# Kernel optimization log

Hardware: AMD Instinct MI355X
Metric: run time of the kernel (lower is better)

## Reference

```python
import jax, jax.numpy as jnp
import numpy as np

B, W, H, A, C, T = 256, 19, 19, 5, 80, 20
DS = 32.0
IOU_THR = 0.5
SCALE_NOOBJ = 0.5
SCALE_OBJ = 5.0
ANCHOR_TRAIN_EPOCHS = 10


def setup_inputs() -> dict:
    key = jax.random.key(0)
    k1, k2, k3, k4, k5, k6 = jax.random.split(key, 6)
    cls_score = jax.random.normal(k1, (B, W, H, A, C), dtype=jnp.float32)
    pred_object = jax.random.normal(k2, (B, W, H, A, 5), dtype=jnp.float32)
    # distinct cells per image -> scatter writes never collide (matches serial loop semantics)
    cell_keys = jax.random.split(k3, B)
    cells = jax.vmap(lambda k: jax.random.permutation(k, W * H)[:T])(cell_keys)  # [B,T]
    ci = (cells // H).astype(jnp.float32)
    cj = (cells % H).astype(jnp.float32)
    off = jax.random.uniform(k4, (B, T, 2), minval=0.2, maxval=0.8)
    wh = jax.random.uniform(k5, (B, T, 2), minval=1.0, maxval=0.9 * W)
    xy = jnp.stack([ci, cj], axis=-1) + off
    true_object = jnp.concatenate([xy, wh], axis=-1) * DS  # image coordinates
    labels = jax.random.randint(k6, (B, T), 0, C)
    true_label = jax.nn.one_hot(labels, C, dtype=jnp.float32)
    # config.anchor_box * fm_width
    anchors = jnp.array([[0.05, 0.07], [0.13, 0.16], [0.22, 0.37], [0.43, 0.26], [0.67, 0.72]],
                        dtype=jnp.float32) * W
    gi, gj = jnp.meshgrid(jnp.arange(W, dtype=jnp.float32), jnp.arange(H, dtype=jnp.float32), indexing='ij')
    fm_cord = jnp.stack([gi, gj], axis=-1)                 # [W,H,2] cell offsets
    fm_size_limit = jnp.full((W, H, 2), float(W), dtype=jnp.float32)
    return {"epoch": 3, "cls_score": cls_score, "pred_object": pred_object,
            "true_object": true_object, "true_label": true_label,
            "anchors": anchors, "fm_cord": fm_cord, "fm_size_limit": fm_size_limit}


def reference(epoch, cls_score, pred_object, true_object, true_label, anchors, fm_cord, fm_size_limit):
    # ---- decode predictions (matches in-place sigmoid decoding) ----
    xy = jax.nn.sigmoid(pred_object[..., :2]) + fm_cord[None, :, :, None, :]
    wh = jax.nn.sigmoid(pred_object[..., 2:4]) * fm_size_limit[None, :, :, None, :]
    conf = jax.nn.sigmoid(pred_object[..., 4])
    pred_dec = jnp.concatenate([xy, wh], axis=-1)          # [B,W,H,A,4]

    # ---- vectorized target assignment (replaces Python b/obj/anchor loops) ----
    to = true_object / DS                                  # [B,T,4] feature-map coords
    ii = jnp.floor(to[..., 0]).astype(jnp.int32)           # [B,T] cell index i
    jj = jnp.floor(to[..., 1]).astype(jnp.int32)           # [B,T] cell index j
    bidx = jnp.arange(B)[:, None]
    pred_cells = pred_dec[bidx, ii, jj]                    # [B,T,A,4] gather

    # center-aligned IoU: only widths/heights matter
    pw, ph = pred_cells[..., 2], pred_cells[..., 3]
    tw, th = to[..., 2][:, :, None], to[..., 3][:, :, None]
    inter = jnp.minimum(pw, tw) * jnp.minimum(ph, th)
    union = pw * ph + tw * th - inter
    iou = inter / union                                    # [B,T,A]
    sel = iou > IOU_THR

    # masked scatter: non-selected rows get an out-of-bounds row index and are dropped
    bb = jnp.broadcast_to(jnp.arange(B)[:, None, None], (B, T, A))
    aa = jnp.broadcast_to(jnp.arange(A)[None, None, :], (B, T, A))
    jj3 = jnp.broadcast_to(jj[:, :, None], (B, T, A))
    ii3 = jnp.where(sel, jnp.broadcast_to(ii[:, :, None], (B, T, A)), W)

    obj_mask = jnp.zeros((B, W, H, A), jnp.float32).at[bb, ii3, jj3, aa].set(1.0, mode='drop')
    iou_buf = jnp.zeros((B, W, H, A), jnp.float32).at[bb, ii3, jj3, aa].set(iou, mode='drop')
    tb_vals = jnp.broadcast_to(to[:, :, None, :], (B, T, A, 4))
    true_bbox = jnp.zeros((B, W, H, A, 4), jnp.float32).at[bb, ii3, jj3, aa].set(tb_vals, mode='drop')
    ts_vals = jnp.broadcast_to(true_label[:, :, None, :], (B, T, A, C))
    true_score = jnp.zeros((B, W, H, A, C), jnp.float32).at[..., -1].set(1.0)
    true_score = true_score.at[bb, ii3, jj3, aa].set(ts_vals, mode='drop')

    # ---- loss terms (MSELoss(reduce=False) == squared error, then mean) ----
    need_prior = 1.0 if epoch < ANCHOR_TRAIN_EPOCHS else 0.0
    noobj_loss = jnp.mean(SCALE_NOOBJ * (1.0 - obj_mask) * 0.5 * conf ** 2)
    obj_loss = jnp.mean(SCALE_OBJ * obj_mask * 0.5 * (conf - iou_buf) ** 2)
    prior_loss = jnp.mean(need_prior * SCALE_OBJ * 0.5 * obj_mask[..., None]
                          * (wh - anchors[None, None, None, :, :]) ** 2)
    true_loss = jnp.mean(SCALE_OBJ * 0.5 * obj_mask[..., None] * (pred_dec - true_bbox) ** 2)
    score_loss = jnp.mean(SCALE_OBJ * 0.5 * (cls_score - true_score) ** 2)
    return (noobj_loss + obj_loss + prior_loss + true_loss + score_loss) / 4.0
```

## Files before the change

### kernel.cpp

```cpp
#include <hip/hip_runtime.h>
#include <math.h>

#define BB 256
#define WD 19
#define HD 19
#define AD 5
#define CD 80
#define TD 20
#define N1 462080
#define NCLS (N1 * CD)
#define NPRED (N1 * 5)

#define NC4 (NCLS / 4)
#define NP4 (NPRED / 4)

#define CLS_BATCHES (NC4 / 1024)
#define PRED_BATCHES (NP4 / 1024)

#define NB_CORR 100
#define NB_CLS  2257
#define NB_PRED 141
#define NBLK (NB_CORR + NB_CLS + NB_PRED)

typedef float f32x4 __attribute__((ext_vector_type(4)));

#define GLOAD(dst, voff, base, imm)                                   \
    asm volatile("global_load_dwordx4 %0, %1, %2 offset:" imm         \
                 : "=v"(dst) : "v"(voff), "s"(base))

__device__ __forceinline__ float sigmoidf_(float x) {
    return 1.0f / (1.0f + expf(-x));
}

#define LOAD_BATCH16(src, b, lane)                                    \
    unsigned o0 = (unsigned)((b) * 1024 + (lane)) * 16u;              \
    unsigned o1 = o0 + 4096u;                                         \
    unsigned o2 = o0 + 8192u;                                         \
    unsigned o3 = o0 + 12288u;                                        \
    f32x4 v0, v1, v2, v3, v4, v5, v6, v7;                             \
    f32x4 v8, v9, v10, v11, v12, v13, v14, v15;                       \
    GLOAD(v0,  o0, src, "0");                                         \
    GLOAD(v1,  o0, src, "1024");                                      \
    GLOAD(v2,  o0, src, "2048");                                      \
    GLOAD(v3,  o0, src, "3072");                                      \
    GLOAD(v4,  o1, src, "0");                                         \
    GLOAD(v5,  o1, src, "1024");                                      \
    GLOAD(v6,  o1, src, "2048");                                      \
    GLOAD(v7,  o1, src, "3072");                                      \
    GLOAD(v8,  o2, src, "0");                                         \
    GLOAD(v9,  o2, src, "1024");                                      \
    GLOAD(v10, o2, src, "2048");                                      \
    GLOAD(v11, o2, src, "3072");                                      \
    GLOAD(v12, o3, src, "0");                                         \
    GLOAD(v13, o3, src, "1024");                                      \
    GLOAD(v14, o3, src, "2048");                                      \
    GLOAD(v15, o3, src, "3072");                                      \
    asm volatile("s_waitcnt vmcnt(0)"                                 \
                 : "+v"(v0), "+v"(v1), "+v"(v2),  "+v"(v3),           \
                   "+v"(v4), "+v"(v5), "+v"(v6),  "+v"(v7),           \
                   "+v"(v8), "+v"(v9), "+v"(v10), "+v"(v11),          \
                   "+v"(v12), "+v"(v13), "+v"(v14), "+v"(v15));

__device__ __forceinline__ void commit_wave(double (*sred)[8], int wib, int lane,
                                            float a0, float a1, float a2, float a3,
                                            float a4, float a5, float a6, float a7) {
    float v[8] = {a0, a1, a2, a3, a4, a5, a6, a7};
    #pragma unroll
    for (int s = 0; s < 8; ++s) {
        #pragma unroll
        for (int off = 32; off > 0; off >>= 1)
            v[s] += __shfl_down(v[s], off, 64);
    }
    if (lane == 0) {
        #pragma unroll
        for (int s = 0; s < 8; ++s) sred[wib][s] = (double)v[s];
    }
}

__global__ void __launch_bounds__(256)
yolo_fused(const float* __restrict__ cls,
           const float* __restrict__ pred,
           const float* __restrict__ tobj,
           const float* __restrict__ tlab,
           const float* __restrict__ anchors,
           const float* __restrict__ fm_cord,
           const float* __restrict__ fm_size,
           double* __restrict__ ws) {
    const int bx = blockIdx.x;
    const int lane = threadIdx.x & 63;
    const int wib = threadIdx.x >> 6;

    __shared__ double sred[4][8];

    if (bx >= NB_CORR && bx < NB_CORR + NB_CLS) {
        const int wave = (bx - NB_CORR) * 4 + wib;
        float sumsq = 0.0f, sum79 = 0.0f;

        if (wave < CLS_BATCHES) {
            const int b = wave;
            LOAD_BATCH16(cls, b, lane);
            const int base20 = (b * 1024 + lane) % 20;
            const f32x4 vv[16] = {v0, v1, v2, v3, v4, v5, v6, v7,
                                  v8, v9, v10, v11, v12, v13, v14, v15};
            #pragma unroll
            for (int k = 0; k < 16; ++k) {
                f32x4 v = vv[k];
                sumsq += v.x * v.x + v.y * v.y + v.z * v.z + v.w * v.w;
                int t = base20 + 4 * k;
                if (t == 19 || t == 39 || t == 59 || t == 79) sum79 += v.w;
            }
        }

        commit_wave(sred, wib, lane, sumsq, sum79, 0.f, 0.f, 0.f, 0.f, 0.f, 0.f);
    } else if (bx >= NB_CORR + NB_CLS) {
        const int wave = (bx - NB_CORR - NB_CLS) * 4 + wib;
        float conf2 = 0.0f;

        {
            const int b = wave;
            LOAD_BATCH16(pred, b, lane);
            const int base5 = (b * 1024 + lane) % 5;
            const f32x4 vv[16] = {v0, v1, v2, v3, v4, v5, v6, v7,
                                  v8, v9, v10, v11, v12, v13, v14, v15};
            #pragma unroll
            for (int k = 0; k < 16; ++k) {
                f32x4 v = vv[k];
                int g5 = (base5 + 4 * k) % 5;
                int kk = (g5 + 4) % 5;
                if (kk < 4) {
                    float x = (kk == 0) ? v.x : (kk == 1) ? v.y
                            : (kk == 2) ? v.z : v.w;
                    float c = sigmoidf_(x);
                    conf2 += c * c;
                }
            }
        }

        if (wave == PRED_BATCHES - 1) {
            int gi = PRED_BATCHES * 1024 + lane;
            float4 v = reinterpret_cast<const float4*>(pred)[gi];
            int kk = (gi + 4) % 5;
            if (kk < 4) {
                float x = (kk == 0) ? v.x : (kk == 1) ? v.y : (kk == 2) ? v.z : v.w;
                float c = sigmoidf_(x);
                conf2 += c * c;
            }
        }

        commit_wave(sred, wib, lane, 0.f, 0.f, conf2, 0.f, 0.f, 0.f, 0.f, 0.f);
    } else {
        const int id = bx * 256 + threadIdx.x;
        float noobj_rm = 0.0f, objs = 0.0f, priors = 0.0f, trues = 0.0f, scorr = 0.0f;

        if (id < BB * TD * AD) {
            int b = id / (TD * AD);
            int r = id % (TD * AD);
            int t = r / AD;
            int a = r % AD;

            const float4 to4 = reinterpret_cast<const float4*>(tobj)[b * TD + t];
            float tox = to4.x * (1.0f / 32.0f);
            float toy = to4.y * (1.0f / 32.0f);
            float tw  = to4.z * (1.0f / 32.0f);
            float th  = to4.w * (1.0f / 32.0f);
            int ii = (int)floorf(tox);
            int jj = (int)floorf(toy);

            const int cell = (b * WD + ii) * HD + jj;
            const float* p = pred + (cell * AD + a) * 5;
            const int fm = (ii * HD + jj) * 2;
            float px = sigmoidf_(p[0]) + fm_cord[fm + 0];
            float py = sigmoidf_(p[1]) + fm_cord[fm + 1];
            float pw = sigmoidf_(p[2]) * fm_size[fm + 0];
            float ph = sigmoidf_(p[3]) * fm_size[fm + 1];
            float conf = sigmoidf_(p[4]);

            float inter = fminf(pw, tw) * fminf(ph, th);
            float uni = pw * ph + tw * th - inter;
            float iou = inter / uni;

            if (iou > 0.5f) {
                noobj_rm = conf * conf;
                objs = (conf - iou) * (conf - iou);
                float aw = anchors[a * 2 + 0];
                float ah = anchors[a * 2 + 1];
                priors = (pw - aw) * (pw - aw) + (ph - ah) * (ph - ah);
                trues = (px - tox) * (px - tox) + (py - toy) * (py - toy)
                      + (pw - tw) * (pw - tw) + (ph - th) * (ph - th);
                const float4* cl4 = reinterpret_cast<const float4*>(cls + (cell * AD + a) * CD);
                const float4* tl4 = reinterpret_cast<const float4*>(tlab + (b * TD + t) * CD);
                float dot = 0.0f;
                float cl79 = 0.0f;
                #pragma unroll 5
                for (int c = 0; c < CD / 4; ++c) {
                    float4 x = cl4[c];
                    float4 y = tl4[c];
                    dot += x.x * y.x + x.y * y.y + x.z * y.z + x.w * y.w;
                    if (c == CD / 4 - 1) cl79 = x.w;
                }
                scorr = 2.0f * cl79 - 2.0f * dot;
            }
        }

        commit_wave(sred, wib, lane, 0.f, 0.f, 0.f, noobj_rm, objs, priors, trues, scorr);
    }

    __syncthreads();
    if (threadIdx.x < 8) {
        ws[bx * 8 + threadIdx.x] = sred[0][threadIdx.x] + sred[1][threadIdx.x]
                                 + sred[2][threadIdx.x] + sred[3][threadIdx.x];
    }
}

__global__ void __launch_bounds__(1024)
yolo_finalize(const double* __restrict__ ws,
              const int* __restrict__ epoch_p,
              float* __restrict__ out) {
    const int lane = threadIdx.x & 63;
    const int wib = threadIdx.x >> 6;
    __shared__ double sh[16][8];

    double acc[8] = {0.0, 0.0, 0.0, 0.0, 0.0, 0.0, 0.0, 0.0};
    for (int b = threadIdx.x; b < NBLK; b += 1024) {
        #pragma unroll
        for (int s = 0; s < 8; ++s) acc[s] += ws[b * 8 + s];
    }
    #pragma unroll
    for (int s = 0; s < 8; ++s) {
        #pragma unroll
        for (int off = 32; off > 0; off >>= 1)
            acc[s] += __shfl_down(acc[s], off, 64);
    }
    if (lane == 0) {
        #pragma unroll
        for (int s = 0; s < 8; ++s) sh[wib][s] = acc[s];
    }
    __syncthreads();

    if (threadIdx.x == 0) {
        double v[8];
        #pragma unroll
        for (int s = 0; s < 8; ++s) {
            double t = 0.0;
            #pragma unroll
            for (int w = 0; w < 16; ++w) t += sh[w][s];
            v[s] = t;
        }

        const double n1 = (double)N1;
        double sumsq = v[0], sum79 = v[1], conf2 = v[2];
        double rm = v[3], objs = v[4], priors = v[5], trues = v[6], scorr = v[7];

        int ev = epoch_p[0];
        double epoch;
        if (ev >= 0 && ev <= 1000000) {
            epoch = (double)ev;
        } else {
            float f = __int_as_float(ev);
            epoch = (double)f;
        }
        double need_prior = (epoch < 10.0) ? 1.0 : 0.0;

        double noobj_loss = 0.25 * (conf2 - rm) / n1;
        double obj_loss   = 2.5 * objs / n1;
        double prior_loss = need_prior * 2.5 * priors / (2.0 * n1);
        double true_loss  = 2.5 * trues / (4.0 * n1);
        double score_base = sumsq + n1 - 2.0 * sum79;
        double score_loss = 2.5 * (score_base + scorr) / (80.0 * n1);

        out[0] = (float)((noobj_loss + obj_loss + prior_loss + true_loss + score_loss) / 4.0);
    }
}

extern "C" void kernel_launch(void* const* d_in, const int* in_sizes, int n_in,
                              void* d_out, int out_size, void* d_ws, size_t ws_size,
                              hipStream_t stream) {
    const int*   epoch   = (const int*)d_in[0];
    const float* cls     = (const float*)d_in[1];
    const float* pred    = (const float*)d_in[2];
    const float* tobj    = (const float*)d_in[3];
    const float* tlab    = (const float*)d_in[4];
    const float* anchors = (const float*)d_in[5];
    const float* fm_cord = (const float*)d_in[6];
    const float* fm_size = (const float*)d_in[7];
    double* ws = (double*)d_ws;
    float* out = (float*)d_out;

    yolo_fused<<<NBLK, 256, 0, stream>>>(
        cls, pred, tobj, tlab, anchors, fm_cord, fm_size, ws);

    yolo_finalize<<<1, 1024, 0, stream>>>(ws, epoch, out);
}
```

Measured before the change: 238.3 us.

## Use persistent waves with double-buffered nontemporal loads for streaming reductions

The one-batch-per-wave launch of the cls and pred streaming sections is replaced by a fixed grid of 512 and 64 blocks. Each wave walks a contiguous range of 512-vector groups and prefetches the next 8 float4 loads while reducing the current ones. Plain nontemporal builtin loads replace the inline asm loads. This cuts block launch and tail overhead and keeps memory requests in flight across iterations, but each wave gets less parallelism per group and depends on the compiler to schedule the loads well.

Measured after the change: 228.5 us. 4.1% less time.

```diff
diff --git a/kernel.cpp b/kernel.cpp
--- a/kernel.cpp
+++ b/kernel.cpp
@@ -14,52 +14,57 @@
 #define NC4 (NCLS / 4)
 #define NP4 (NPRED / 4)
 
-#define CLS_BATCHES (NC4 / 1024)
-#define PRED_BATCHES (NP4 / 1024)
+#define CLS_GROUPS (NC4 / 512)
+#define PRED_GROUPS (NP4 / 512)
 
 #define NB_CORR 100
-#define NB_CLS  2257
-#define NB_PRED 141
+#define NB_CLS  512
+#define NB_PRED 64
 #define NBLK (NB_CORR + NB_CLS + NB_PRED)
+#define CLS_WAVES_T (NB_CLS * 4)
+#define PRED_WAVES_T (NB_PRED * 4)
 
 typedef float f32x4 __attribute__((ext_vector_type(4)));
-
-#define GLOAD(dst, voff, base, imm)                                   \
-    asm volatile("global_load_dwordx4 %0, %1, %2 offset:" imm         \
-                 : "=v"(dst) : "v"(voff), "s"(base))
 
 __device__ __forceinline__ float sigmoidf_(float x) {
     return 1.0f / (1.0f + expf(-x));
 }
 
-#define LOAD_BATCH16(src, b, lane)                                    \
-    unsigned o0 = (unsigned)((b) * 1024 + (lane)) * 16u;              \
-    unsigned o1 = o0 + 4096u;                                         \
-    unsigned o2 = o0 + 8192u;                                         \
-    unsigned o3 = o0 + 12288u;                                        \
-    f32x4 v0, v1, v2, v3, v4, v5, v6, v7;                             \
-    f32x4 v8, v9, v10, v11, v12, v13, v14, v15;                       \
-    GLOAD(v0,  o0, src, "0");                                         \
-    GLOAD(v1,  o0, src, "1024");                                      \
-    GLOAD(v2,  o0, src, "2048");                                      \
-    GLOAD(v3,  o0, src, "3072");                                      \
-    GLOAD(v4,  o1, src, "0");                                         \
-    GLOAD(v5,  o1, src, "1024");                                      \
-    GLOAD(v6,  o1, src, "2048");                                      \
-    GLOAD(v7,  o1, src, "3072");                                      \
-    GLOAD(v8,  o2, src, "0");                                         \
-    GLOAD(v9,  o2, src, "1024");                                      \
-    GLOAD(v10, o2, src, "2048");                                      \
-    GLOAD(v11, o2, src, "3072");                                      \
-    GLOAD(v12, o3, src, "0");                                         \
-    GLOAD(v13, o3, src, "1024");                                      \
-    GLOAD(v14, o3, src, "2048");                                      \
-    GLOAD(v15, o3, src, "3072");                                      \
-    asm volatile("s_waitcnt vmcnt(0)"                                 \
-                 : "+v"(v0), "+v"(v1), "+v"(v2),  "+v"(v3),           \
-                   "+v"(v4), "+v"(v5), "+v"(v6),  "+v"(v7),           \
-                   "+v"(v8), "+v"(v9), "+v"(v10), "+v"(v11),          \
-                   "+v"(v12), "+v"(v13), "+v"(v14), "+v"(v15));
+__device__ __forceinline__ void load8(f32x4 (&d)[8], const f32x4* __restrict__ s4,
+                                      int g, int lane) {
+    #pragma unroll
+    for (int k = 0; k < 8; ++k)
+        d[k] = __builtin_nontemporal_load(s4 + (size_t)g * 512 + (size_t)(k * 64 + lane));
+}
+
+__device__ __forceinline__ void consume_cls(const f32x4 (&v)[8], int g, int lane,
+                                            float& sumsq, float& sum79) {
+    const int base20 = (g * 512 + lane) % 20;
+    #pragma unroll
+    for (int k = 0; k < 8; ++k) {
+        f32x4 q = v[k];
+        sumsq += q.x * q.x + q.y * q.y + q.z * q.z + q.w * q.w;
+        int t = base20 + 4 * k;
+        if (t == 19 || t == 39) sum79 += q.w;
+    }
+}
+
+__device__ __forceinline__ void consume_pred(const f32x4 (&v)[8], int g, int lane,
+                                             float& conf2) {
+    const int base5 = (g * 512 + lane) % 5;
+    #pragma unroll
+    for (int k = 0; k < 8; ++k) {
+        f32x4 q = v[k];
+        int g5 = base5 + ((4 * k) % 5);
+        if (g5 >= 5) g5 -= 5;
+        if (g5 != 0) {
+            int kk = g5 - 1;
+            float x = (kk == 0) ? q.x : (kk == 1) ? q.y : (kk == 2) ? q.z : q.w;
+            float c = sigmoidf_(x);
+            conf2 += c * c;
+        }
+    }
+}
 
 __device__ __forceinline__ void commit_wave(double (*sred)[8], int wib, int lane,
                                             float a0, float a1, float a2, float a3,
@@ -94,50 +99,43 @@
 
     if (bx >= NB_CORR && bx < NB_CORR + NB_CLS) {
         const int wave = (bx - NB_CORR) * 4 + wib;
+        const int g0 = (int)(((long long)wave * CLS_GROUPS) / CLS_WAVES_T);
+        const int g1 = (int)(((long long)(wave + 1) * CLS_GROUPS) / CLS_WAVES_T);
+
         float sumsq = 0.0f, sum79 = 0.0f;
-
-        if (wave < CLS_BATCHES) {
-            const int b = wave;
-            LOAD_BATCH16(cls, b, lane);
-            const int base20 = (b * 1024 + lane) % 20;
-            const f32x4 vv[16] = {v0, v1, v2, v3, v4, v5, v6, v7,
-                                  v8, v9, v10, v11, v12, v13, v14, v15};
+        const f32x4* c4 = reinterpret_cast<const f32x4*>(cls);
+
+        f32x4 cur[8], nxt[8];
+        load8(cur, c4, g0, lane);
+        for (int g = g0 + 1; g < g1; ++g) {
+            load8(nxt, c4, g, lane);
+            consume_cls(cur, g - 1, lane, sumsq, sum79);
             #pragma unroll
-            for (int k = 0; k < 16; ++k) {
-                f32x4 v = vv[k];
-                sumsq += v.x * v.x + v.y * v.y + v.z * v.z + v.w * v.w;
-                int t = base20 + 4 * k;
-                if (t == 19 || t == 39 || t == 59 || t == 79) sum79 += v.w;
-            }
-        }
+            for (int k = 0; k < 8; ++k) cur[k] = nxt[k];
+        }
+        consume_cls(cur, g1 - 1, lane, sumsq, sum79);
 
         commit_wave(sred, wib, lane, sumsq, sum79, 0.f, 0.f, 0.f, 0.f, 0.f, 0.f);
     } else if (bx >= NB_CORR + NB_CLS) {
         const int wave = (bx - NB_CORR - NB_CLS) * 4 + wib;
+        const int g0 = (int)(((long long)wave * PRED_GROUPS) / PRED_WAVES_T);
+        const int g1 = (int)(((long long)(wave + 1) * PRED_GROUPS) / PRED_WAVES_T);
+
         float conf2 = 0.0f;
-
-        {
-            const int b = wave;
-            LOAD_BATCH16(pred, b, lane);
-            const int base5 = (b * 1024 + lane) % 5;
-            const f32x4 vv[16] = {v0, v1, v2, v3, v4, v5, v6, v7,
-                                  v8, v9, v10, v11, v12, v13, v14, v15};
+        const f32x4* p4 = reinterpret_cast<const f32x4*>(pred);
+
+        f32x4 cur[8], nxt[8];
+        load8(cur, p4, g0, lane);
+        for (int g = g0 + 1; g < g1; ++g) {
+            load8(nxt, p4, g, lane);
+            consume_pred(cur, g - 1, lane, conf2);
             #pragma unroll
-            for (int k = 0; k < 16; ++k) {
-                f32x4 v = vv[k];
-                int g5 = (base5 + 4 * k) % 5;
-                int kk = (g5 + 4) % 5;
-                if (kk < 4) {
-                    float x = (kk == 0) ? v.x : (kk == 1) ? v.y
-                            : (kk == 2) ? v.z : v.w;
-                    float c = sigmoidf_(x);
-                    conf2 += c * c;
-                }
-            }
-        }
-
-        if (wave == PRED_BATCHES - 1) {
-            int gi = PRED_BATCHES * 1024 + lane;
+            for (int k = 0; k < 8; ++k) cur[k] = nxt[k];
+        }
+        consume_pred(cur, g1 - 1, lane, conf2);
+
+        if (wave == PRED_WAVES_T - 1) {
+            int gi = PRED_GROUPS * 512 + lane;
             float4 v = reinterpret_cast<const float4*>(pred)[gi];
             int kk = (gi + 4) % 5;
             if (kk < 4) {
```
